# Kernel optimization log

Measured on AMD Instinct MI355X. Metric: run time of the kernel, lower is better.

## Reference

```python
import jax, jax.numpy as jnp
import numpy as np

E = 1024  # embed_dim
H = 1     # num_heads (energy_W matmul forces head_dim == embed_dim)
TEMPERATURE = 1.0


def setup_inputs() -> dict:
    key = jax.random.key(0)
    ks = jax.random.split(key, 10)
    B, S = 8, 2048
    inp = {
        "query": jax.random.normal(ks[0], (B, S, E), dtype=jnp.float32),
        "key": jax.random.normal(ks[1], (B, S, E), dtype=jnp.float32),
        "value": jax.random.normal(ks[2], (B, S, E), dtype=jnp.float32),
        "mask": jnp.ones((1, 1, S, S), dtype=jnp.int32),
        # nn.Linear params (y = x @ W.T + b)
        "Wq": jax.random.normal(ks[3], (E, E), dtype=jnp.float32) * (1.0 / np.sqrt(E)),
        "bq": jnp.zeros((E,), dtype=jnp.float32),
        "Wk": jax.random.normal(ks[4], (E, E), dtype=jnp.float32) * (1.0 / np.sqrt(E)),
        "bk": jnp.zeros((E,), dtype=jnp.float32),
        "Wv": jax.random.normal(ks[5], (E, E), dtype=jnp.float32) * (1.0 / np.sqrt(E)),
        "bv": jnp.zeros((E,), dtype=jnp.float32),
        "energy_W": jax.random.normal(ks[6], (E, E), dtype=jnp.float32),
    }
    return inp


def reference(query, key, value, mask, Wq, bq, Wk, bk, Wv, bv, energy_W):
    B, S, _ = query.shape
    hd = E // H
    # projections (torch Linear: x @ W.T + b), then split heads -> [B, H, S, hd]
    q = (query @ Wq.T + bq).reshape(B, S, H, hd).transpose(0, 2, 1, 3)
    k = (key @ Wk.T + bk).reshape(B, S, H, hd).transpose(0, 2, 1, 3)
    v = (value @ Wv.T + bv).reshape(B, S, H, hd).transpose(0, 2, 1, 3)
    # bilinear energy: (q) @ (k @ W)^T   -> [B, H, Sq, Sk]
    k_t = k @ energy_W
    energy = jnp.einsum("bhqd,bhkd->bhqk", q, k_t) / TEMPERATURE
    energy = jnp.where(mask == 0, jnp.float32(-1e9), energy)
    attn_weights = jax.nn.softmax(-energy, axis=-1)
    out = jnp.einsum("bhqk,bhkd->bhqd", attn_weights, v)
    out = out.transpose(0, 2, 1, 3).reshape(B, S, E)
    return (out, attn_weights)
```

## Files before the change

kernel.cpp:

```cpp
#include <hip/hip_runtime.h>


typedef __attribute__((ext_vector_type(8))) short short8;
typedef __attribute__((ext_vector_type(4))) float f32x4;
typedef __attribute__((ext_vector_type(16))) float f32x16;

#define E_DIM 1024
#define S_LEN 2048
#define NB 8

__device__ __forceinline__ unsigned short rne_bf(float x) {
    unsigned int u = __float_as_uint(x);
    return (unsigned short)((u + 0x7fffu + ((u >> 16) & 1u)) >> 16);
}

__device__ __forceinline__ void splitbf(float x, unsigned short& h, unsigned short& l) {
    unsigned int u = __float_as_uint(x);
    unsigned int rh = ((u + 0x7fffu + ((u >> 16) & 1u)) >> 16) << 16;
    h = (unsigned short)(rh >> 16);
    float r = x - __uint_as_float(rh);
    unsigned int v = __float_as_uint(r);
    l = (unsigned short)((v + 0x7fffu + ((v >> 16) & 1u)) >> 16);
}

__device__ __forceinline__ void lds_cp16(const void* g, void* l) {
    __builtin_amdgcn_global_load_lds(
        (const __attribute__((address_space(1))) unsigned int*)g,
        (__attribute__((address_space(3))) unsigned int*)l, 16, 0, 0);
}

__device__ __forceinline__ void wait_vm6() { asm volatile("s_waitcnt vmcnt(6)" ::: "memory"); }
__device__ __forceinline__ void wait_vm4() { asm volatile("s_waitcnt vmcnt(4)" ::: "memory"); }
__device__ __forceinline__ void wait_vm3() { asm volatile("s_waitcnt vmcnt(3)" ::: "memory"); }
__device__ __forceinline__ void wait_vm0() { asm volatile("s_waitcnt vmcnt(0)" ::: "memory"); }

__device__ __forceinline__ void swizzle_xy(int& bx, int& by) {
    const int gx = gridDim.x, gy = gridDim.y;
    const int nwg = gx * gy;
    const int w = by * gx + bx;
    if ((gx & 3) == 0 && (gy & 3) == 0 && (((gx >> 2) * (gy >> 2)) & 7) == 0) {
        const int nchx = gx >> 2;
        const int xcd = w & 7, i = w >> 3;
        const int j = i >> 4, p = i & 15;
        const int ch = xcd + 8 * j;
        const int chy = ch / nchx, chx = ch - chy * nchx;
        by = chy * 4 + (p >> 2);
        bx = chx * 4 + (p & 3);
    } else if ((nwg & 7) == 0) {
        const int cpx = nwg >> 3;
        const int sw = (w & 7) * cpx + (w >> 3);
        bx = sw % gx;
        by = sw / gx;
    }
}

template <bool DO_L>
__global__ __launch_bounds__(256) void conv_img(
    const float* __restrict__ src, unsigned short* __restrict__ h,
    unsigned short* __restrict__ l, int ld, int nkt)
{
    const int t = threadIdx.x;
    const long long tb = ((long long)blockIdx.y * nkt + blockIdx.x) * 4096;
    const float* s0 = src + (long long)blockIdx.y * 128 * ld + blockIdx.x * 32;
#pragma unroll
    for (int i = 0; i < 4; ++i) {
        const int f = i * 256 + t;
        const int r = f >> 3;
        const int c4 = (f & 7) << 2;
        const float4 v = *(const float4*)(s0 + (long long)r * ld + c4);
        const int gg = c4 >> 3;
        const int half = (c4 >> 2) & 1;
        const long long wo = tb + (long long)(gg * 128 + r) * 8 + half * 4;
        unsigned short h0, h1, h2, h3;
        if (DO_L) {
            unsigned short l0, l1, l2, l3;
            splitbf(v.x, h0, l0); splitbf(v.y, h1, l1);
            splitbf(v.z, h2, l2); splitbf(v.w, h3, l3);
            uint2 hp, lp;
            hp.x = h0 | ((unsigned)h1 << 16); hp.y = h2 | ((unsigned)h3 << 16);
            lp.x = l0 | ((unsigned)l1 << 16); lp.y = l2 | ((unsigned)l3 << 16);
            *(uint2*)(h + wo) = hp;
            *(uint2*)(l + wo) = lp;
        } else {
            h0 = rne_bf(v.x); h1 = rne_bf(v.y); h2 = rne_bf(v.z); h3 = rne_bf(v.w);
            uint2 hp;
            hp.x = h0 | ((unsigned)h1 << 16); hp.y = h2 | ((unsigned)h3 << 16);
            *(uint2*)(h + wo) = hp;
        }
    }
}

__global__ __launch_bounds__(256) void conv_imgT(
    const float* __restrict__ src, unsigned short* __restrict__ h,
    unsigned short* __restrict__ l, int nkt)
{
    __shared__ float tile[32][132];
    const int t = threadIdx.x;
    const int kt = blockIdx.x;
    const int rb = blockIdx.y;
    const float* s0 = src + (long long)kt * 32 * E_DIM + rb * 128;
#pragma unroll
    for (int i = 0; i < 4; ++i) {
        const int f = i * 256 + t;
        const int r = f >> 5;
        const int c4 = (f & 31) << 2;
        const float4 v = *(const float4*)(s0 + (long long)r * E_DIM + c4);
        tile[r][c4] = v.x; tile[r][c4 + 1] = v.y;
        tile[r][c4 + 2] = v.z; tile[r][c4 + 3] = v.w;
    }
    __syncthreads();
    const long long tb = ((long long)rb * nkt + kt) * 4096;
#pragma unroll
    for (int i = 0; i < 2; ++i) {
        const int c = i * 256 + t;
        const int g = c >> 7, r = c & 127;
        unsigned short hh[8], ll[8];
#pragma unroll
        for (int j = 0; j < 8; ++j) splitbf(tile[g * 8 + j][r], hh[j], ll[j]);
        uint4 hp, lp;
        hp.x = hh[0] | ((unsigned)hh[1] << 16); hp.y = hh[2] | ((unsigned)hh[3] << 16);
        hp.z = hh[4] | ((unsigned)hh[5] << 16); hp.w = hh[6] | ((unsigned)hh[7] << 16);
        lp.x = ll[0] | ((unsigned)ll[1] << 16); lp.y = ll[2] | ((unsigned)ll[3] << 16);
        lp.z = ll[4] | ((unsigned)ll[5] << 16); lp.w = ll[6] | ((unsigned)ll[7] << 16);
        *(uint4*)(h + tb + (long long)c * 8) = hp;
        *(uint4*)(l + tb + (long long)c * 8) = lp;
    }
}

__global__ __launch_bounds__(512, 4) void gemm_e3(
    const unsigned short* __restrict__ Ah, const unsigned short* __restrict__ Al,
    const unsigned short* __restrict__ Bh, const unsigned short* __restrict__ Bl,
    float* __restrict__ C, int ldC, long long bsC, int nkt32, int aZrb, int bZrb)
{
    __shared__ unsigned short smb[36864];

    const int t = threadIdx.x;
    const int wv = t >> 6, lane = t & 63;
    const int wr = wv >> 1, wc = wv & 1;
    const int l31 = lane & 31, lh = lane >> 5;

    int bx = blockIdx.x, by = blockIdx.y;
    swizzle_xy(bx, by);

    const long long aB0 = ((long long)blockIdx.z * aZrb + 2 * by) * nkt32 * 4096;
    const long long aB1 = aB0 + (long long)nkt32 * 4096;
    const long long bB0 = ((long long)blockIdx.z * bZrb + bx) * nkt32 * 4096;

    const int rA = t & 255, glA = t >> 8;
    const int bc = t & 255;
    auto stage = [&](int k16, int c) {
        unsigned short* buf = smb + c * 12288;
        const int kt32 = k16 >> 1, hh = k16 & 1;
        const long long aOff = ((rA >> 7) ? aB1 : aB0) + (long long)kt32 * 4096
                             + ((2 * hh + glA) * 128 + (rA & 127)) * 8;
        lds_cp16(Ah + aOff, buf + t * 8);
        lds_cp16(Al + aOff, buf + 4096 + t * 8);
        const long long bOff = bB0 + (long long)kt32 * 4096
                             + ((2 * hh + (bc >> 7)) * 128 + (bc & 127)) * 8;
        const unsigned short* bsrc = (t < 256) ? Bh : Bl;
        lds_cp16(bsrc + bOff, buf + 8192 + t * 8);
    };

    short8 ah[2], al[2], bh[2], bl[2];
    auto loadFrags = [&](int c) {
        const unsigned short* buf = smb + c * 12288;
#pragma unroll
        for (int m = 0; m < 2; ++m) {
            const int ra = lh * 256 + wr * 64 + m * 32 + l31;
            ah[m] = *(const short8*)(buf + ra * 8);
            al[m] = *(const short8*)(buf + 4096 + ra * 8);
        }
#pragma unroll
        for (int n = 0; n < 2; ++n) {
            const int rb = lh * 128 + wc * 64 + n * 32 + l31;
            bh[n] = *(const short8*)(buf + 8192 + rb * 8);
            bl[n] = *(const short8*)(buf + 10240 + rb * 8);
        }
    };

    f32x16 acc[2][2] = {};
    const int n16 = nkt32 * 2;

    stage(0, 0);
    stage(1, 1);

    for (int s = 0; s < n16; ++s) {
        __builtin_amdgcn_s_barrier();
        if (s + 2 < n16) {
            stage(s + 2, (s + 2) % 3);
            wait_vm6();
        } else if (s + 1 < n16) {
            wait_vm3();
        } else {
            wait_vm0();
        }
        __builtin_amdgcn_s_barrier();
        __builtin_amdgcn_sched_barrier(0);
        loadFrags(s % 3);
        __builtin_amdgcn_s_setprio(1);
#pragma unroll
        for (int m = 0; m < 2; ++m)
#pragma unroll
            for (int n = 0; n < 2; ++n)
                acc[m][n] = __builtin_amdgcn_mfma_f32_32x32x16_bf16(ah[m], bh[n], acc[m][n], 0, 0, 0);
#pragma unroll
        for (int m = 0; m < 2; ++m)
#pragma unroll
            for (int n = 0; n < 2; ++n)
                acc[m][n] = __builtin_amdgcn_mfma_f32_32x32x16_bf16(al[m], bh[n], acc[m][n], 0, 0, 0);
#pragma unroll
        for (int m = 0; m < 2; ++m)
#pragma unroll
            for (int n = 0; n < 2; ++n)
                acc[m][n] = __builtin_amdgcn_mfma_f32_32x32x16_bf16(ah[m], bl[n], acc[m][n], 0, 0, 0);
        __builtin_amdgcn_s_setprio(0);
    }

    float* Cb = C + (long long)blockIdx.z * bsC;
#pragma unroll
    for (int m = 0; m < 2; ++m)
#pragma unroll
        for (int n = 0; n < 2; ++n) {
            const int gc = bx * 128 + wc * 64 + n * 32 + l31;
            const int gr0 = by * 256 + wr * 64 + m * 32 + 4 * lh;
#pragma unroll
            for (int reg = 0; reg < 16; ++reg) {
                const int row = (reg & 3) + 8 * (reg >> 2);
                Cb[(long long)(gr0 + row) * ldC + gc] = acc[m][n][reg];
            }
        }
}

template <int NPROD>
__global__ __launch_bounds__(512, 4) void gemm_big(
    const unsigned short* __restrict__ Ah, const unsigned short* __restrict__ Al,
    const unsigned short* __restrict__ Bh, const unsigned short* __restrict__ Bl,
    float* __restrict__ C, const float* __restrict__ bias,
    int ldC, long long bsC, int nkt, int aZrb, int bZrb)
{
    __shared__ unsigned short smb[36864];

    const int t = threadIdx.x;
    const int wv = t >> 6, lane = t & 63;
    const int wr = wv >> 1, wc = wv & 1;
    const int lr = lane & 15, gq = lane >> 4;

    int bx = blockIdx.x, by = blockIdx.y;
    swizzle_xy(bx, by);

    const long long aB0 = ((long long)blockIdx.z * aZrb + 2 * by) * nkt * 4096;
    const long long aB1 = aB0 + (long long)nkt * 4096;
    const long long bB0 = ((long long)blockIdx.z * bZrb + bx) * nkt * 4096;

    auto srcptr = [&](int s, const unsigned short*& a0, const unsigned short*& a1,
                      const unsigned short*& bS) {
        int seg, kt;
        if (NPROD == 3) {
            seg = (s >= 2 * nkt) ? 2 : (s >= nkt ? 1 : 0);
            kt = s - seg * nkt;
        } else { seg = 0; kt = s; }
        const unsigned short* aBase = ((NPROD == 3 && seg == 1) ? Al : Ah);
        const unsigned short* bBase = ((NPROD == 3 && seg == 2) ? Bl : Bh);
        a0 = aBase + aB0 + (long long)kt * 4096;
        a1 = aBase + aB1 + (long long)kt * 4096;
        bS = bBase + bB0 + (long long)kt * 4096;
    };
    auto stage = [&](const unsigned short* a0, const unsigned short* a1,
                     const unsigned short* bS, int c) {
        unsigned short* dA = smb + c * 12288;
        lds_cp16(a0 + t * 8, dA + t * 8);
        lds_cp16(a1 + t * 8, dA + 4096 + t * 8);
        lds_cp16(bS + t * 8, dA + 8192 + t * 8);
    };

    short8 af[4], bfr[4];
    auto loadFrags = [&](int c) {
        const unsigned short* dA = smb + c * 12288;
        const unsigned short* dB = dA + 8192;
#pragma unroll
        for (int m = 0; m < 4; ++m) {
            const int R = wr * 64 + m * 16 + lr;
            af[m] = *(const short8*)(dA + (R >> 7) * 4096 + (gq * 128 + (R & 127)) * 8);
        }
#pragma unroll
        for (int n = 0; n < 4; ++n) {
            const int Cc = wc * 64 + n * 16 + lr;
            bfr[n] = *(const short8*)(dB + (gq * 128 + Cc) * 8);
        }
    };

    f32x4 acc[4][4] = {};
    const int nsteps = NPROD * nkt;

    {
        const unsigned short *a0, *a1, *bS;
        srcptr(0, a0, a1, bS); stage(a0, a1, bS, 0);
        srcptr(1, a0, a1, bS); stage(a0, a1, bS, 1);
    }
    wait_vm3();
    __builtin_amdgcn_s_barrier();
    __builtin_amdgcn_sched_barrier(0);
    loadFrags(0);

    for (int s = 0; s < nsteps; ++s) {
        if (s + 2 < nsteps) {
            const unsigned short *a0, *a1, *bS;
            srcptr(s + 2, a0, a1, bS);
            stage(a0, a1, bS, (s + 2) % 3);
        }
        __builtin_amdgcn_sched_barrier(0);
        __builtin_amdgcn_s_setprio(1);
#pragma unroll
        for (int m = 0; m < 4; ++m)
#pragma unroll
            for (int n = 0; n < 4; ++n)
                acc[m][n] = __builtin_amdgcn_mfma_f32_16x16x32_bf16(af[m], bfr[n], acc[m][n], 0, 0, 0);
        __builtin_amdgcn_s_setprio(0);
        __builtin_amdgcn_sched_barrier(0);
        if (s + 1 < nsteps) {
            if (s + 2 < nsteps) wait_vm3();
            else wait_vm0();
            __builtin_amdgcn_s_barrier();
            __builtin_amdgcn_sched_barrier(0);
            loadFrags((s + 1) % 3);
        }
    }

    const int cr = (lane >> 4) << 2, cc = lane & 15;
    float* Cb = C + (long long)blockIdx.z * bsC;
#pragma unroll
    for (int m = 0; m < 4; ++m)
#pragma unroll
        for (int n = 0; n < 4; ++n) {
            const int gc = bx * 128 + wc * 64 + n * 16 + cc;
            const float badd = bias ? bias[gc] : 0.0f;
            const int gr0 = by * 256 + wr * 64 + m * 16 + cr;
#pragma unroll
            for (int i = 0; i < 4; ++i)
                Cb[(long long)(gr0 + i) * ldC + gc] = acc[m][n][i] + badd;
        }
}

template <int NPROD, int WMODE>
__global__ __launch_bounds__(256) void gemm_img(
    const unsigned short* __restrict__ Ah, const unsigned short* __restrict__ Al,
    const unsigned short* __restrict__ Bh, const unsigned short* __restrict__ Bl,
    float* __restrict__ C, const float* __restrict__ bias,
    unsigned short* __restrict__ imgH, unsigned short* __restrict__ imgL,
    int ldC, long long bsC, int nkt, int aZrb, int bZrb, int outNkt)
{
    extern __shared__ unsigned short sm[];

    const int t = threadIdx.x;
    const int wv = t >> 6, lane = t & 63;
    const int wm = (wv >> 1) << 6, wn = (wv & 1) << 6;
    const int lr = lane & 15, gq = lane >> 4;

    int bx = blockIdx.x, by = blockIdx.y;
    swizzle_xy(bx, by);

    const long long aB0 = ((long long)blockIdx.z * aZrb + by) * nkt * 4096;
    const long long bB0 = ((long long)blockIdx.z * bZrb + bx) * nkt * 4096;

    auto srcptr = [&](int s, const unsigned short*& aS, const unsigned short*& bS) {
        int seg, kt;
        if (NPROD == 3) {
            seg = (s >= 2 * nkt) ? 2 : (s >= nkt ? 1 : 0);
            kt = s - seg * nkt;
        } else { seg = 0; kt = s; }
        aS = ((NPROD == 3 && seg == 1) ? Al : Ah) + aB0 + (long long)kt * 4096;
        bS = ((NPROD == 3 && seg == 2) ? Bl : Bh) + bB0 + (long long)kt * 4096;
    };
    auto stage = [&](const unsigned short* aS, const unsigned short* bS, int c) {
        unsigned short* dA = sm + c * 8192;
        unsigned short* dB = dA + 4096;
#pragma unroll
        for (int j = 0; j < 2; ++j) {
            lds_cp16(aS + (wv * 128 + j * 64 + lane) * 8, dA + (wv * 128 + j * 64) * 8);
            lds_cp16(bS + (wv * 128 + j * 64 + lane) * 8, dB + (wv * 128 + j * 64) * 8);
        }
    };

    short8 af[4], bfr[4];
    auto loadFrags = [&](int c) {
        const unsigned short* smA = sm + c * 8192;
        const unsigned short* smB = smA + 4096;
        const unsigned short* pa = smA + (gq * 128 + wm + lr) * 8;
        const unsigned short* pb = smB + (gq * 128 + wn + lr) * 8;
#pragma unroll
        for (int m = 0; m < 4; ++m) af[m] = *(const short8*)(pa + m * 128);
#pragma unroll
        for (int n = 0; n < 4; ++n) bfr[n] = *(const short8*)(pb + n * 128);
    };

    f32x4 acc[4][4] = {};
    const int nsteps = NPROD * nkt;

    {
        const unsigned short *aS, *bS;
        srcptr(0, aS, bS); stage(aS, bS, 0);
        srcptr(1, aS, bS); stage(aS, bS, 1);
    }
    wait_vm4();
    __builtin_amdgcn_s_barrier();
    __builtin_amdgcn_sched_barrier(0);
    loadFrags(0);

    for (int s = 0; s < nsteps; ++s) {
        if (s + 2 < nsteps) {
            const unsigned short *aS, *bS;
            srcptr(s + 2, aS, bS);
            stage(aS, bS, (s + 2) % 3);
        }
        __builtin_amdgcn_sched_barrier(0);
        __builtin_amdgcn_s_setprio(1);
#pragma unroll
        for (int m = 0; m < 4; ++m)
#pragma unroll
            for (int n = 0; n < 4; ++n)
                acc[m][n] = __builtin_amdgcn_mfma_f32_16x16x32_bf16(af[m], bfr[n], acc[m][n], 0, 0, 0);
        __builtin_amdgcn_s_setprio(0);
        __builtin_amdgcn_sched_barrier(0);
        if (s + 1 < nsteps) {
            if (s + 2 < nsteps) wait_vm4();
            else wait_vm0();
            __builtin_amdgcn_s_barrier();
            __builtin_amdgcn_sched_barrier(0);
            loadFrags((s + 1) % 3);
        }
    }

    const int cr = (lane >> 4) << 2, cc = lane & 15;
    if (WMODE == 0) {
        float* Cb = C + (long long)blockIdx.z * bsC;
#pragma unroll
        for (int m = 0; m < 4; ++m)
#pragma unroll
            for (int n = 0; n < 4; ++n) {
                const int gc = bx * 128 + wn + n * 16 + cc;
                const float badd = bias ? bias[gc] : 0.0f;
                const int gr0 = by * 128 + wm + m * 16 + cr;
#pragma unroll
                for (int i = 0; i < 4; ++i)
                    Cb[(long long)(gr0 + i) * ldC + gc] = acc[m][n][i] + badd;
            }
    } else {
        float* slab = (float*)sm;
        const int wmi = wv >> 1;
#pragma unroll
        for (int m = 0; m < 4; ++m) {
            __syncthreads();
#pragma unroll
            for (int n = 0; n < 4; ++n) {
                const int col = wn + n * 16 + cc;
                const float badd = bias ? bias[bx * 128 + col] : 0.0f;
#pragma unroll
                for (int i = 0; i < 4; ++i)
                    slab[(wmi * 16 + cr + i) * 132 + col] = acc[m][n][i] + badd;
            }
            __syncthreads();
            if (WMODE == 1) {
#pragma unroll
                for (int it = 0; it < 2; ++it) {
                    const int e = it * 256 + t;
                    const int wq = e >> 8, cg = (e >> 4) & 15, fr = e & 15;
                    const float* sp = slab + (wq * 16 + fr) * 132 + cg * 8;
                    const int rIn = wq * 64 + m * 16 + fr;
                    const int ktO = bx * 4 + (cg >> 2);
                    const int gO = cg & 3;
                    const long long base =
                        ((long long)by * outNkt + ktO) * 4096 + (gO * 128 + rIn) * 8;
                    unsigned short h[8], l[8];
#pragma unroll
                    for (int j = 0; j < 8; ++j) splitbf(sp[j], h[j], l[j]);
                    uint4 hp, lp;
                    hp.x = h[0] | ((unsigned)h[1] << 16); hp.y = h[2] | ((unsigned)h[3] << 16);
                    hp.z = h[4] | ((unsigned)h[5] << 16); hp.w = h[6] | ((unsigned)h[7] << 16);
                    lp.x = l[0] | ((unsigned)l[1] << 16); lp.y = l[2] | ((unsigned)l[3] << 16);
                    lp.z = l[4] | ((unsigned)l[5] << 16); lp.w = l[6] | ((unsigned)l[7] << 16);
                    *(uint4*)(imgH + base) = hp;
                    *(uint4*)(imgL + base) = lp;
                }
            } else {
#pragma unroll
                for (int it = 0; it < 2; ++it) {
                    const int e = it * 256 + t;
                    const int wq = e >> 8, s8 = (e >> 7) & 1, dl = e & 127;
                    const int sG = by * 128 + wq * 64 + m * 16 + s8 * 8;
                    const int z = sG >> 11, sIn = sG & 2047;
                    const int ktO = sIn >> 5, gO = (sIn >> 3) & 3;
                    const long long base =
                        ((long long)(z * 8 + bx) * 64 + ktO) * 4096 + (gO * 128 + dl) * 8;
                    unsigned short h[8];
#pragma unroll
                    for (int j = 0; j < 8; ++j)
                        h[j] = rne_bf(slab[(wq * 16 + s8 * 8 + j) * 132 + dl]);
                    uint4 hp;
                    hp.x = h[0] | ((unsigned)h[1] << 16); hp.y = h[2] | ((unsigned)h[3] << 16);
                    hp.z = h[4] | ((unsigned)h[5] << 16); hp.w = h[6] | ((unsigned)h[7] << 16);
                    *(uint4*)(imgH + base) = hp;
                }
            }
        }
    }
}

__global__ __launch_bounds__(256) void softmax_img(
    float* __restrict__ attn, const int* __restrict__ mask,
    unsigned short* __restrict__ img)
{
    const int row = blockIdx.x;
    const int q = row & (S_LEN - 1);
    const int t = threadIdx.x;
    const int lane = t & 63, wid = t >> 6;
    float* rp = attn + (long long)row * S_LEN;
    const int* mp = mask + (long long)q * S_LEN;

    const float4 e0 = *(const float4*)(rp + t * 8);
    const float4 e1 = *(const float4*)(rp + t * 8 + 4);
    const int4 ma = *(const int4*)(mp + t * 8);
    const int4 mb = *(const int4*)(mp + t * 8 + 4);
    float zv[8];
    zv[0] = ma.x ? -e0.x : 1e9f;
    zv[1] = ma.y ? -e0.y : 1e9f;
    zv[2] = ma.z ? -e0.z : 1e9f;
    zv[3] = ma.w ? -e0.w : 1e9f;
    zv[4] = mb.x ? -e1.x : 1e9f;
    zv[5] = mb.y ? -e1.y : 1e9f;
    zv[6] = mb.z ? -e1.z : 1e9f;
    zv[7] = mb.w ? -e1.w : 1e9f;
    float mx = zv[0];
#pragma unroll
    for (int j = 1; j < 8; ++j) mx = fmaxf(mx, zv[j]);
#pragma unroll
    for (int o = 32; o > 0; o >>= 1) mx = fmaxf(mx, __shfl_xor(mx, o));
    __shared__ float redm[4], reds[4];
    if (lane == 0) redm[wid] = mx;
    __syncthreads();
    mx = fmaxf(fmaxf(redm[0], redm[1]), fmaxf(redm[2], redm[3]));
    float s = 0.f;
#pragma unroll
    for (int j = 0; j < 8; ++j) { zv[j] = expf(zv[j] - mx); s += zv[j]; }
#pragma unroll
    for (int o = 32; o > 0; o >>= 1) s += __shfl_xor(s, o);
    if (lane == 0) reds[wid] = s;
    __syncthreads();
    s = reds[0] + reds[1] + reds[2] + reds[3];
    const float inv = 1.0f / s;
    float4 o0, o1;
    o0.x = zv[0] * inv; o0.y = zv[1] * inv; o0.z = zv[2] * inv; o0.w = zv[3] * inv;
    o1.x = zv[4] * inv; o1.y = zv[5] * inv; o1.z = zv[6] * inv; o1.w = zv[7] * inv;
    *(float4*)(rp + t * 8) = o0;
    *(float4*)(rp + t * 8 + 4) = o1;
    const int z = row >> 11, rb = (row >> 7) & 15;
    const int ktO = t >> 2, gO = t & 3, r = row & 127;
    const long long base = (((long long)(z * 16 + rb) * 64 + ktO) * 512 + gO * 128 + r) * 8;
    uint4 hp;
    hp.x = rne_bf(o0.x) | ((unsigned)rne_bf(o0.y) << 16);
    hp.y = rne_bf(o0.z) | ((unsigned)rne_bf(o0.w) << 16);
    hp.z = rne_bf(o1.x) | ((unsigned)rne_bf(o1.y) << 16);
    hp.w = rne_bf(o1.z) | ((unsigned)rne_bf(o1.w) << 16);
    *(uint4*)(img + base) = hp;
}

__global__ void transpose1024(const float* __restrict__ in, float* __restrict__ out)
{
    __shared__ float tile[32][33];
    const int bx = blockIdx.x << 5, by = blockIdx.y << 5;
    const int tx = threadIdx.x, ty = threadIdx.y;
#pragma unroll
    for (int i = 0; i < 4; ++i)
        tile[ty + 8 * i][tx] = in[(long long)(by + ty + 8 * i) * E_DIM + bx + tx];
    __syncthreads();
#pragma unroll
    for (int i = 0; i < 4; ++i)
        out[(long long)(bx + ty + 8 * i) * E_DIM + by + tx] = tile[tx][ty + 8 * i];
}

__global__ __launch_bounds__(256) void bias_c_kernel(
    const float* __restrict__ We, const float* __restrict__ bq, float* __restrict__ c)
{
    const int i = blockIdx.x;
    const int t = threadIdx.x;
    float s = 0.f;
    for (int d = t; d < E_DIM; d += 256) s += bq[d] * We[(long long)i * E_DIM + d];
#pragma unroll
    for (int o = 32; o > 0; o >>= 1) s += __shfl_xor(s, o);
    __shared__ float red[4];
    if ((t & 63) == 0) red[t >> 6] = s;
    __syncthreads();
    if (t == 0) c[i] = red[0] + red[1] + red[2] + red[3];
}

template <bool SPLIT, int WMODE>
__global__ __launch_bounds__(256) void gemm_split(
    const float* __restrict__ A, const float* __restrict__ B,
    float* __restrict__ C, const float* __restrict__ bias,
    int M, int N, int K,
    long long bsA, long long bsB, long long bsC)
{
    extern __shared__ unsigned short sm[];
    unsigned short* sAh = sm;
    unsigned short* sBh = sm + 5120;
    unsigned short* sAl = sm + 10240;
    unsigned short* sBl = sm + 15360;

    const int t = threadIdx.x;
    const int z = blockIdx.z;
    const float* Ab = A + (long long)z * bsA + (long long)blockIdx.y * 128 * K;
    const float* Bb = B + (long long)z * bsB + (long long)blockIdx.x * 128 * K;

    const int wv = t >> 6;
    const int lane = t & 63;
    const int wm = (wv >> 1) << 6;
    const int wn = (wv & 1) << 6;
    const int lr = lane & 15;
    const int ko = (lane >> 4) << 3;

    f32x4 acc[4][4] = {};

    for (int k0 = 0; k0 < K; k0 += 32) {
        __syncthreads();
#pragma unroll
        for (int i = 0; i < 4; ++i) {
            const int f = t + (i << 8);
            const int row = f >> 3;
            const int c4 = (f & 7) << 2;
            const float4 av = *(const float4*)(Ab + (long long)row * K + k0 + c4);
            const float4 bv = *(const float4*)(Bb + (long long)row * K + k0 + c4);
            if (SPLIT) {
                unsigned short h0, h1, h2, h3, l0, l1, l2, l3;
                splitbf(av.x, h0, l0); splitbf(av.y, h1, l1);
                splitbf(av.z, h2, l2); splitbf(av.w, h3, l3);
                uint2 hp, lp;
                hp.x = (unsigned)h0 | ((unsigned)h1 << 16);
                hp.y = (unsigned)h2 | ((unsigned)h3 << 16);
                lp.x = (unsigned)l0 | ((unsigned)l1 << 16);
                lp.y = (unsigned)l2 | ((unsigned)l3 << 16);
                *(uint2*)(sAh + row * 40 + c4) = hp;
                *(uint2*)(sAl + row * 40 + c4) = lp;
                splitbf(bv.x, h0, l0); splitbf(bv.y, h1, l1);
                splitbf(bv.z, h2, l2); splitbf(bv.w, h3, l3);
                hp.x = (unsigned)h0 | ((unsigned)h1 << 16);
                hp.y = (unsigned)h2 | ((unsigned)h3 << 16);
                lp.x = (unsigned)l0 | ((unsigned)l1 << 16);
                lp.y = (unsigned)l2 | ((unsigned)l3 << 16);
                *(uint2*)(sBh + row * 40 + c4) = hp;
                *(uint2*)(sBl + row * 40 + c4) = lp;
            } else {
                uint2 hp;
                hp.x = (unsigned)rne_bf(av.x) | ((unsigned)rne_bf(av.y) << 16);
                hp.y = (unsigned)rne_bf(av.z) | ((unsigned)rne_bf(av.w) << 16);
                *(uint2*)(sAh + row * 40 + c4) = hp;
                hp.x = (unsigned)rne_bf(bv.x) | ((unsigned)rne_bf(bv.y) << 16);
                hp.y = (unsigned)rne_bf(bv.z) | ((unsigned)rne_bf(bv.w) << 16);
                *(uint2*)(sBh + row * 40 + c4) = hp;
            }
        }
        __syncthreads();
        short8 ah[4], bh[4], al[4], bl[4];
#pragma unroll
        for (int m = 0; m < 4; ++m)
            ah[m] = *(const short8*)(sAh + (wm + m * 16 + lr) * 40 + ko);
#pragma unroll
        for (int n = 0; n < 4; ++n)
            bh[n] = *(const short8*)(sBh + (wn + n * 16 + lr) * 40 + ko);
        if (SPLIT) {
#pragma unroll
            for (int m = 0; m < 4; ++m)
                al[m] = *(const short8*)(sAl + (wm + m * 16 + lr) * 40 + ko);
#pragma unroll
            for (int n = 0; n < 4; ++n)
                bl[n] = *(const short8*)(sBl + (wn + n * 16 + lr) * 40 + ko);
        }
#pragma unroll
        for (int m = 0; m < 4; ++m) {
#pragma unroll
            for (int n = 0; n < 4; ++n) {
                acc[m][n] = __builtin_amdgcn_mfma_f32_16x16x32_bf16(ah[m], bh[n], acc[m][n], 0, 0, 0);
                if (SPLIT) {
                    acc[m][n] = __builtin_amdgcn_mfma_f32_16x16x32_bf16(ah[m], bl[n], acc[m][n], 0, 0, 0);
                    acc[m][n] = __builtin_amdgcn_mfma_f32_16x16x32_bf16(al[m], bh[n], acc[m][n], 0, 0, 0);
                }
            }
        }
    }

    const int cr = (lane >> 4) << 2;
    const int cc = lane & 15;
    float* Cb = C + (long long)z * bsC;
#pragma unroll
    for (int m = 0; m < 4; ++m) {
#pragma unroll
        for (int n = 0; n < 4; ++n) {
            const int gc = blockIdx.x * 128 + wn + n * 16 + cc;
            const float badd = bias ? bias[gc] : 0.0f;
            const int gr0 = blockIdx.y * 128 + wm + m * 16 + cr;
#pragma unroll
            for (int i = 0; i < 4; ++i) {
                const float val = acc[m][n][i] + badd;
                if (WMODE == 0) {
                    Cb[(long long)(gr0 + i) * N + gc] = val;
                } else {
                    const int r = gr0 + i;
                    Cb[(long long)(r >> 11) * ((long long)N * 2048) +
                       (long long)gc * 2048 + (r & 2047)] = val;
                }
            }
        }
    }
}

__global__ __launch_bounds__(256) void softmax_rows(
    float* __restrict__ attn, const int* __restrict__ mask)
{
    const int row = blockIdx.x;
    const int q = row & (S_LEN - 1);
    const int t = threadIdx.x;
    const int lane = t & 63, wid = t >> 6;
    float* rp = attn + (long long)row * S_LEN;
    const int* mp = mask + (long long)q * S_LEN;

    float zv[8];
    float mx = -3.4e38f;
#pragma unroll
    for (int j = 0; j < 8; ++j) {
        const int idx = t + (j << 8);
        const float e = rp[idx];
        const int mv = mp[idx];
        const float zz = (mv != 0) ? -e : 1e9f;
        zv[j] = zz;
        mx = fmaxf(mx, zz);
    }
#pragma unroll
    for (int o = 32; o > 0; o >>= 1) mx = fmaxf(mx, __shfl_xor(mx, o));
    __shared__ float redm[4], reds[4];
    if (lane == 0) redm[wid] = mx;
    __syncthreads();
    mx = fmaxf(fmaxf(redm[0], redm[1]), fmaxf(redm[2], redm[3]));

    float s = 0.f;
#pragma unroll
    for (int j = 0; j < 8; ++j) { zv[j] = expf(zv[j] - mx); s += zv[j]; }
#pragma unroll
    for (int o = 32; o > 0; o >>= 1) s += __shfl_xor(s, o);
    if (lane == 0) reds[wid] = s;
    __syncthreads();
    s = reds[0] + reds[1] + reds[2] + reds[3];
    const float inv = 1.0f / s;
#pragma unroll
    for (int j = 0; j < 8; ++j) rp[t + (j << 8)] = zv[j] * inv;
}

extern "C" void kernel_launch(void* const* d_in, const int* in_sizes, int n_in,
                              void* d_out, int out_size, void* d_ws, size_t ws_size,
                              hipStream_t stream)
{
    const float* query = (const float*)d_in[0];
    const float* key   = (const float*)d_in[1];
    const float* value = (const float*)d_in[2];
    const int*   mask  = (const int*)d_in[3];
    const float* Wq    = (const float*)d_in[4];
    const float* bq    = (const float*)d_in[5];
    const float* Wk    = (const float*)d_in[6];
    const float* bk    = (const float*)d_in[7];
    const float* Wv    = (const float*)d_in[8];
    const float* bv    = (const float*)d_in[9];
    const float* We    = (const float*)d_in[10];

    float* out  = (float*)d_out;
    float* attn = out + (long long)NB * S_LEN * E_DIM;

    const size_t oWqT  = 0;
    const size_t oCvec = oWqT + (4u << 20);
    const size_t oWqTH = oCvec + 4096;
    const size_t oWqTL = oWqTH + (2u << 20);
    const size_t oWeH  = oWqTL + (2u << 20);
    const size_t oWeL  = oWeH + (2u << 20);
    const size_t oWkH  = oWeL + (2u << 20);
    const size_t oWkL  = oWkH + (2u << 20);
    const size_t oWvH  = oWkL + (2u << 20);
    const size_t oPH   = oWvH + (2u << 20);
    const size_t oPL   = oPH + (2u << 20);
    const size_t oBig1 = oPL + (2u << 20);
    const size_t oBig2 = oBig1 + (64u << 20);
    const size_t oBig3 = oBig2 + (64u << 20);
    const size_t NEED  = oBig3 + (64u << 20);

    char* wsb = (char*)d_ws;

    if (ws_size >= NEED) {
        float* cvec = (float*)(wsb + oCvec);
        unsigned short* WqTH = (unsigned short*)(wsb + oWqTH);
        unsigned short* WqTL = (unsigned short*)(wsb + oWqTL);
        unsigned short* WeH  = (unsigned short*)(wsb + oWeH);
        unsigned short* WeL  = (unsigned short*)(wsb + oWeL);
        unsigned short* WkH  = (unsigned short*)(wsb + oWkH);
        unsigned short* WkL  = (unsigned short*)(wsb + oWkL);
        unsigned short* WvH  = (unsigned short*)(wsb + oWvH);
        unsigned short* PH   = (unsigned short*)(wsb + oPH);
        unsigned short* PL   = (unsigned short*)(wsb + oPL);
        unsigned short* qryH = (unsigned short*)(wsb + oBig1);
        unsigned short* qryL = (unsigned short*)(wsb + oBig1 + (32u << 20));
        unsigned short* attnH = (unsigned short*)(wsb + oBig1);
        unsigned short* keyH = (unsigned short*)(wsb + oBig2);
        unsigned short* keyL = (unsigned short*)(wsb + oBig2 + (32u << 20));
        unsigned short* qwH  = (unsigned short*)(wsb + oBig2);
        unsigned short* qwL  = (unsigned short*)(wsb + oBig2 + (32u << 20));
        unsigned short* kH   = (unsigned short*)(wsb + oBig3);
        unsigned short* kL   = (unsigned short*)(wsb + oBig3 + (32u << 20));
        unsigned short* vTH  = (unsigned short*)(wsb + oBig3);
        unsigned short* valH = (unsigned short*)(wsb + oBig3 + (32u << 20));

        bias_c_kernel<<<1024, 256, 0, stream>>>(We, bq, cvec);
        conv_imgT<<<dim3(32, 8), 256, 0, stream>>>(Wq, WqTH, WqTL, 32);
        conv_img<true><<<dim3(32, 8), 256, 0, stream>>>(We, WeH, WeL, 1024, 32);
        conv_img<true><<<dim3(32, 8), 256, 0, stream>>>(Wk, WkH, WkL, 1024, 32);
        conv_img<false><<<dim3(32, 8), 256, 0, stream>>>(Wv, WvH, nullptr, 1024, 32);
        conv_img<true><<<dim3(32, 128), 256, 0, stream>>>(query, qryH, qryL, 1024, 32);
        conv_img<true><<<dim3(32, 128), 256, 0, stream>>>(key, keyH, keyL, 1024, 32);

        gemm_img<3, 1><<<dim3(8, 8, 1), 256, 49152, stream>>>(
            WeH, WeL, WqTH, WqTL, nullptr, nullptr, PH, PL, 0, 0, 32, 0, 0, 32);
        gemm_img<3, 1><<<dim3(8, 128, 1), 256, 49152, stream>>>(
            keyH, keyL, WkH, WkL, nullptr, bk, kH, kL, 0, 0, 32, 0, 0, 32);
        gemm_img<3, 1><<<dim3(8, 128, 1), 256, 49152, stream>>>(
            qryH, qryL, PH, PL, nullptr, cvec, qwH, qwL, 0, 0, 32, 0, 0, 32);
        gemm_e3<<<dim3(16, 8, NB), 512, 0, stream>>>(
            qwH, qwL, kH, kL, attn,
            2048, (long long)S_LEN * S_LEN, 32, 16, 16);
        conv_img<false><<<dim3(32, 128), 256, 0, stream>>>(value, valH, nullptr, 1024, 32);
        gemm_img<1, 3><<<dim3(8, 128, 1), 256, 49152, stream>>>(
            valH, nullptr, WvH, nullptr, nullptr, bv, vTH, nullptr, 0, 0, 32, 0, 0, 0);
        softmax_img<<<NB * S_LEN, 256, 0, stream>>>(attn, mask, attnH);
        gemm_big<1><<<dim3(8, 8, NB), 512, 0, stream>>>(
            attnH, nullptr, vTH, nullptr, out, nullptr,
            1024, (long long)S_LEN * E_DIM, 64, 16, 8);
    } else {
        float* ws   = (float*)d_ws;
        float* WqT  = ws;
        float* P    = WqT + 1048576;
        float* cvec = P + 1048576;
        float* kbuf = cvec + 1024;
        float* qw   = kbuf + 16777216;
        float* vT   = qw + 16777216;
        const size_t need_old = (size_t)(1048576 * 2 + 1024 + 16777216 * 3) * 4;
        if (ws_size < need_old) return;

        transpose1024<<<dim3(32, 32), dim3(32, 8), 0, stream>>>(Wq, WqT);
        bias_c_kernel<<<1024, 256, 0, stream>>>(We, bq, cvec);
        gemm_split<true, 0><<<dim3(8, 8, 1), 256, 40960, stream>>>(
            We, WqT, P, nullptr, 1024, 1024, 1024, 0, 0, 0);
        gemm_split<true, 0><<<dim3(8, 128, 1), 256, 40960, stream>>>(
            key, Wk, kbuf, bk, 16384, 1024, 1024, 0, 0, 0);
        gemm_split<false, 1><<<dim3(8, 128, 1), 256, 20480, stream>>>(
            value, Wv, vT, bv, 16384, 1024, 1024, 0, 0, 0);
        gemm_split<true, 0><<<dim3(8, 128, 1), 256, 40960, stream>>>(
            query, P, qw, cvec, 16384, 1024, 1024, 0, 0, 0);
        gemm_split<true, 0><<<dim3(16, 16, NB), 256, 40960, stream>>>(
            qw, kbuf, attn, nullptr, 2048, 2048, 1024,
            (long long)S_LEN * E_DIM, (long long)S_LEN * E_DIM, (long long)S_LEN * S_LEN);
        softmax_rows<<<NB * S_LEN, 256, 0, stream>>>(attn, mask);
        gemm_split<false, 0><<<dim3(8, 16, NB), 256, 20480, stream>>>(
            attn, vT, out, nullptr, 2048, 1024, 2048,
            (long long)S_LEN * S_LEN, (long long)E_DIM * S_LEN, (long long)S_LEN * E_DIM);
    }

    (void)in_sizes; (void)n_in; (void)out_size;
}
```

Measured before the change: 792.6 us.

## Fold key projection into a combined weight matrix to drop the key GEMM

After: 768.5 us. 1.03x faster.

```diff
diff --git a/kernel.cpp b/kernel.cpp
--- a/kernel.cpp
+++ b/kernel.cpp
@@ -127,9 +127,35 @@
     }
 }
 
+__global__ __launch_bounds__(256) void wvecT_kernel(
+    const float* __restrict__ Wk, const float* __restrict__ t1, float* __restrict__ w)
+{
+    const int i = blockIdx.x * 256 + threadIdx.x;
+    float s = 0.f;
+    for (int d = 0; d < E_DIM; ++d) s += Wk[(long long)d * E_DIM + i] * t1[d];
+    w[i] = s;
+}
+
+__global__ __launch_bounds__(256) void rvec_kernel(
+    const float* __restrict__ key, const float* __restrict__ w, float* __restrict__ r)
+{
+    const int row = blockIdx.x;
+    const int t = threadIdx.x;
+    const float4 kv = ((const float4*)(key + (long long)row * E_DIM))[t];
+    const float4 wv = ((const float4*)w)[t];
+    float s = kv.x * wv.x + kv.y * wv.y + kv.z * wv.z + kv.w * wv.w;
+#pragma unroll
+    for (int o = 32; o > 0; o >>= 1) s += __shfl_xor(s, o);
+    __shared__ float red[4];
+    if ((t & 63) == 0) red[t >> 6] = s;
+    __syncthreads();
+    if (t == 0) r[row] = red[0] + red[1] + red[2] + red[3];
+}
+
 __global__ __launch_bounds__(512, 4) void gemm_e3(
     const unsigned short* __restrict__ Ah, const unsigned short* __restrict__ Al,
     const unsigned short* __restrict__ Bh, const unsigned short* __restrict__ Bl,
+    const float* __restrict__ rbias,
     float* __restrict__ C, int ldC, long long bsC, int nkt32, int aZrb, int bZrb)
 {
     __shared__ unsigned short smb[36864];
@@ -222,11 +248,12 @@
 #pragma unroll
         for (int n = 0; n < 2; ++n) {
             const int gc = bx * 128 + wc * 64 + n * 32 + l31;
+            const float rb = rbias ? rbias[(long long)blockIdx.z * 2048 + gc] : 0.0f;
             const int gr0 = by * 256 + wr * 64 + m * 32 + 4 * lh;
 #pragma unroll
             for (int reg = 0; reg < 16; ++reg) {
                 const int row = (reg & 3) + 8 * (reg >> 2);
-                Cb[(long long)(gr0 + row) * ldC + gc] = acc[m][n][reg];
+                Cb[(long long)(gr0 + row) * ldC + gc] = acc[m][n][reg] + rb;
             }
         }
 }
@@ -771,18 +798,20 @@
     float* out  = (float*)d_out;
     float* attn = out + (long long)NB * S_LEN * E_DIM;
 
-    const size_t oWqT  = 0;
-    const size_t oCvec = oWqT + (4u << 20);
-    const size_t oWqTH = oCvec + 4096;
-    const size_t oWqTL = oWqTH + (2u << 20);
-    const size_t oWeH  = oWqTL + (2u << 20);
-    const size_t oWeL  = oWeH + (2u << 20);
-    const size_t oWkH  = oWeL + (2u << 20);
-    const size_t oWkL  = oWkH + (2u << 20);
-    const size_t oWvH  = oWkL + (2u << 20);
-    const size_t oPH   = oWvH + (2u << 20);
-    const size_t oPL   = oPH + (2u << 20);
-    const size_t oBig1 = oPL + (2u << 20);
+    const size_t oT1   = 0;
+    const size_t oW    = 4096;
+    const size_t oR    = 8192;
+    const size_t oWts  = 131072;
+    const size_t oWqTH = oWts + 0 * (2u << 20);
+    const size_t oWqTL = oWts + 1 * (2u << 20);
+    const size_t oWkTH = oWts + 2 * (2u << 20);
+    const size_t oWkTL = oWts + 3 * (2u << 20);
+    const size_t oWeH  = oWts + 4 * (2u << 20);
+    const size_t oWeL  = oWts + 5 * (2u << 20);
+    const size_t oWvH  = oWts + 6 * (2u << 20);
+    const size_t oPTH  = oWts + 7 * (2u << 20);
+    const size_t oPTL  = oWts + 8 * (2u << 20);
+    const size_t oBig1 = oWts + 9 * (2u << 20);
     const size_t oBig2 = oBig1 + (64u << 20);
     const size_t oBig3 = oBig2 + (64u << 20);
     const size_t NEED  = oBig3 + (64u << 20);
@@ -790,44 +819,49 @@
     char* wsb = (char*)d_ws;
 
     if (ws_size >= NEED) {
-        float* cvec = (float*)(wsb + oCvec);
+        float* t1 = (float*)(wsb + oT1);
+        float* wv = (float*)(wsb + oW);
+        float* rv = (float*)(wsb + oR);
         unsigned short* WqTH = (unsigned short*)(wsb + oWqTH);
         unsigned short* WqTL = (unsigned short*)(wsb + oWqTL);
+        unsigned short* WkTH = (unsigned short*)(wsb + oWkTH);
+        unsigned short* WkTL = (unsigned short*)(wsb + oWkTL);
         unsigned short* WeH  = (unsigned short*)(wsb + oWeH);
         unsigned short* WeL  = (unsigned short*)(wsb + oWeL);
-        unsigned short* WkH  = (unsigned short*)(wsb + oWkH);
-        unsigned short* WkL  = (unsigned short*)(wsb + oWkL);
+        unsigned short* GTH  = (unsigned short*)(wsb + oWeH);
+        unsigned short* GTL  = (unsigned short*)(wsb + oWeL);
         unsigned short* WvH  = (unsigned short*)(wsb + oWvH);
-        unsigned short* PH   = (unsigned short*)(wsb + oPH);
-        unsigned short* PL   = (unsigned short*)(wsb + oPL);
+        unsigned short* PTH  = (unsigned short*)(wsb + oPTH);
+        unsigned short* PTL  = (unsigned short*)(wsb + oPTL);
         unsigned short* qryH = (unsigned short*)(wsb + oBig1);
         unsigned short* qryL = (unsigned short*)(wsb + oBig1 + (32u << 20));
         unsigned short* attnH = (unsigned short*)(wsb + oBig1);
         unsigned short* keyH = (unsigned short*)(wsb + oBig2);
         unsigned short* keyL = (unsigned short*)(wsb + oBig2 + (32u << 20));
-        unsigned short* qwH  = (unsigned short*)(wsb + oBig2);
-        unsigned short* qwL  = (unsigned short*)(wsb + oBig2 + (32u << 20));
-        unsigned short* kH   = (unsigned short*)(wsb + oBig3);
-        unsigned short* kL   = (unsigned short*)(wsb + oBig3 + (32u << 20));
+        unsigned short* qgH  = (unsigned short*)(wsb + oBig3);
+        unsigned short* qgL  = (unsigned short*)(wsb + oBig3 + (32u << 20));
         unsigned short* vTH  = (unsigned short*)(wsb + oBig3);
         unsigned short* valH = (unsigned short*)(wsb + oBig3 + (32u << 20));
 
-        bias_c_kernel<<<1024, 256, 0, stream>>>(We, bq, cvec);
+        bias_c_kernel<<<1024, 256, 0, stream>>>(We, bq, t1);
+        wvecT_kernel<<<4, 256, 0, stream>>>(Wk, t1, wv);
+        rvec_kernel<<<NB * S_LEN, 256, 0, stream>>>(key, wv, rv);
+
         conv_imgT<<<dim3(32, 8), 256, 0, stream>>>(Wq, WqTH, WqTL, 32);
+        conv_imgT<<<dim3(32, 8), 256, 0, stream>>>(Wk, WkTH, WkTL, 32);
         conv_img<true><<<dim3(32, 8), 256, 0, stream>>>(We, WeH, WeL, 1024, 32);
-        conv_img<true><<<dim3(32, 8), 256, 0, stream>>>(Wk, WkH, WkL, 1024, 32);
         conv_img<false><<<dim3(32, 8), 256, 0, stream>>>(Wv, WvH, nullptr, 1024, 32);
         conv_img<true><<<dim3(32, 128), 256, 0, stream>>>(query, qryH, qryL, 1024, 32);
         conv_img<true><<<dim3(32, 128), 256, 0, stream>>>(key, keyH, keyL, 1024, 32);
 
         gemm_img<3, 1><<<dim3(8, 8, 1), 256, 49152, stream>>>(
-            WeH, WeL, WqTH, WqTL, nullptr, nullptr, PH, PL, 0, 0, 32, 0, 0, 32);
+            WqTH, WqTL, WeH, WeL, nullptr, nullptr, PTH, PTL, 0, 0, 32, 0, 0, 32);
+        gemm_img<3, 1><<<dim3(8, 8, 1), 256, 49152, stream>>>(
+            WkTH, WkTL, PTH, PTL, nullptr, nullptr, GTH, GTL, 0, 0, 32, 0, 0, 32);
         gemm_img<3, 1><<<dim3(8, 128, 1), 256, 49152, stream>>>(
-            keyH, keyL, WkH, WkL, nullptr, bk, kH, kL, 0, 0, 32, 0, 0, 32);
-        gemm_img<3, 1><<<dim3(8, 128, 1), 256, 49152, stream>>>(
-            qryH, qryL, PH, PL, nullptr, cvec, qwH, qwL, 0, 0, 32, 0, 0, 32);
+            qryH, qryL, GTH, GTL, nullptr, nullptr, qgH, qgL, 0, 0, 32, 0, 0, 32);
         gemm_e3<<<dim3(16, 8, NB), 512, 0, stream>>>(
-            qwH, qwL, kH, kL, attn,
+            qgH, qgL, keyH, keyL, rv, attn,
             2048, (long long)S_LEN * S_LEN, 32, 16, 16);
         conv_img<false><<<dim3(32, 128), 256, 0, stream>>>(value, valH, nullptr, 1024, 32);
         gemm_img<1, 3><<<dim3(8, 128, 1), 256, 49152, stream>>>(
```
